# Kernel tuning notes

Hardware: AMD Instinct MI355X
Metric: run time of the kernel (lower is better)

Reference implementation:

```python
import jax, jax.numpy as jnp
import numpy as np

BATCH = 4096
IN_DIM = 2048      # pooled CNN feature dim
OUT_DIM = 14951    # landmark classes
EPS = 1e-12        # tf.nn.l2_normalize epsilon


def _hadamard_slice(rows, cols):
    # Sylvester Hadamard entry: H[i, j] = (-1)^popcount(i & j).
    # Builds only the [rows, cols] slice of the 16384x16384 matrix.
    i = jnp.arange(rows, dtype=jnp.uint32)[:, None]
    j = jnp.arange(cols, dtype=jnp.uint32)[None, :]
    par = jax.lax.population_count(i & j) & 1
    return 1.0 - 2.0 * par.astype(jnp.float32)


def setup_inputs() -> dict:
    key = jax.random.key(0)
    k1, k2 = jax.random.split(key)
    x = jax.random.normal(k1, (BATCH, IN_DIM), dtype=jnp.float32)
    init_scale = 1.0 / np.sqrt(OUT_DIM)
    scale = jnp.full((1,), init_scale, dtype=jnp.float32)
    bias = jax.random.uniform(k2, (OUT_DIM,), dtype=jnp.float32,
                              minval=-init_scale, maxval=init_scale)
    return {"x": x, "scale": scale, "bias": bias}


def reference(x, scale, bias):
    H = _hadamard_slice(x.shape[1], bias.shape[0])  # [IN_DIM, OUT_DIM], +-1
    # L2-normalize along last axis (matches K.l2_normalize / tf.nn.l2_normalize)
    xn = x * jax.lax.rsqrt(jnp.maximum(jnp.sum(x * x, axis=-1, keepdims=True), EPS))
    out = -scale * jnp.matmul(xn, H) + bias  # activation=None
    return out
```

## Files before the change

### kernel.cpp

```cpp
#include <hip/hip_runtime.h>

#define BATCH   4096
#define IN_DIM  2048
#define OUT_DIM 14951
#define ROWS    4
#define NT      512
#define STRIDE  2052
#define EPS     1e-12f

__global__ __launch_bounds__(NT, 8) void HadamardClassifier_44487271252814_kernel(
    const float* __restrict__ x,
    const float* __restrict__ scale,
    const float* __restrict__ bias,
    float* __restrict__ out)
{
    __shared__ float y[ROWS * STRIDE];
    __shared__ float rss[ROWS * 2];
    __shared__ float srow[ROWS];

    const int tid = threadIdx.x;
    const int r   = tid >> 7;
    const int t   = tid & 127;
    const int b0  = blockIdx.x * ROWS;

    const float4* xv = reinterpret_cast<const float4*>(x + (size_t)(b0 + r) * IN_DIM) + 4 * t;
    float4 v0 = xv[0], v1 = xv[1], v2 = xv[2], v3 = xv[3];
    float a[16] = { v0.x, v0.y, v0.z, v0.w, v1.x, v1.y, v1.z, v1.w,
                    v2.x, v2.y, v2.z, v2.w, v3.x, v3.y, v3.z, v3.w };

    float ss = 0.f;
    #pragma unroll
    for (int k = 0; k < 16; ++k) ss += a[k] * a[k];
    #pragma unroll
    for (int o = 32; o > 0; o >>= 1) ss += __shfl_down(ss, o, 64);
    if ((tid & 63) == 0) rss[tid >> 6] = ss;

    #pragma unroll
    for (int h = 1; h < 16; h <<= 1) {
        #pragma unroll
        for (int g = 0; g < 16; g += 2 * h) {
            #pragma unroll
            for (int k = 0; k < h; ++k) {
                float u = a[g + k], w = a[g + k + h];
                a[g + k]     = u + w;
                a[g + k + h] = u - w;
            }
        }
    }

    float* yr = y + r * STRIDE;
    #pragma unroll
    for (int k = 0; k < 4; ++k) {
        *reinterpret_cast<float4*>(&yr[16 * t + 4 * k]) =
            make_float4(a[4 * k], a[4 * k + 1], a[4 * k + 2], a[4 * k + 3]);
    }
    __syncthreads();

    if (tid < ROWS)
        srow[tid] = -scale[0] * rsqrtf(fmaxf(rss[2 * tid] + rss[2 * tid + 1], EPS));

    #pragma unroll
    for (int h = 16; h < IN_DIM; h <<= 1) {
        #pragma unroll
        for (int q = 0; q < 2; ++q) {
            int idx = 4 * (t + 128 * q);
            int i = ((idx & ~(h - 1)) << 1) | (idx & (h - 1));
            float4 u = *reinterpret_cast<float4*>(&yr[i]);
            float4 w = *reinterpret_cast<float4*>(&yr[i + h]);
            float4 su, sw;
            su.x = u.x + w.x; su.y = u.y + w.y; su.z = u.z + w.z; su.w = u.w + w.w;
            sw.x = u.x - w.x; sw.y = u.y - w.y; sw.z = u.z - w.z; sw.w = u.w - w.w;
            *reinterpret_cast<float4*>(&yr[i])     = su;
            *reinterpret_cast<float4*>(&yr[i + h]) = sw;
        }
        __syncthreads();
    }

    float4* obase = reinterpret_cast<float4*>(out + (size_t)b0 * OUT_DIM);
    const int NF4 = (ROWS * OUT_DIM) / 4;

    for (int f4 = tid; f4 < NF4; f4 += NT) {
        int e  = f4 << 2;
        int rr = (e >= OUT_DIM) + (e >= 2 * OUT_DIM) + (e >= 3 * OUT_DIM);
        int j  = e - rr * OUT_DIM;
        float4 o;
        if (j + 3 < OUT_DIM) {
            float sv = srow[rr];
            const float* yq = y + rr * STRIDE;
            int m = j & (IN_DIM - 1);
            float y0 = yq[m];
            float y1 = yq[(m + 1) & (IN_DIM - 1)];
            float y2 = yq[(m + 2) & (IN_DIM - 1)];
            float y3 = yq[(m + 3) & (IN_DIM - 1)];
            o.x = fmaf(sv, y0, bias[j]);
            o.y = fmaf(sv, y1, bias[j + 1]);
            o.z = fmaf(sv, y2, bias[j + 2]);
            o.w = fmaf(sv, y3, bias[j + 3]);
        } else {
            float tmp[4];
            #pragma unroll
            for (int c = 0; c < 4; ++c) {
                int ee = e + c;
                int rc = (ee >= OUT_DIM) + (ee >= 2 * OUT_DIM) + (ee >= 3 * OUT_DIM);
                int jc = ee - rc * OUT_DIM;
                tmp[c] = fmaf(srow[rc], y[rc * STRIDE + (jc & (IN_DIM - 1))], bias[jc]);
            }
            o = make_float4(tmp[0], tmp[1], tmp[2], tmp[3]);
        }
        obase[f4] = o;
    }
}

extern "C" void kernel_launch(void* const* d_in, const int* in_sizes, int n_in,
                              void* d_out, int out_size, void* d_ws, size_t ws_size,
                              hipStream_t stream) {
    const float* x     = (const float*)d_in[0];
    const float* scale = (const float*)d_in[1];
    const float* bias  = (const float*)d_in[2];
    float* out = (float*)d_out;

    hipLaunchKernelGGL(HadamardClassifier_44487271252814_kernel,
                       dim3(BATCH / ROWS), dim3(NT), 0, stream,
                       x, scale, bias, out);
}
```

Baseline: 288.8 us.

## Use wave shuffles for FWHT stages and vectorize row-aligned output stores

Replaces the shared-memory butterfly stages h=16..1024 with in-register shfl_xor stages across the wavefront and a single shared-memory exchange for the final stage. This cuts the number of block barriers. The output loop is restructured so each iteration writes four aligned float4s, one per row, with per-row shifted reads of the transform and bias. It uses nontemporal stores and handles the few misaligned edge elements separately. The rewrite is meant to remove the scalar LDS gathers, the per-element row/column index math, and the cache pollution caused by the large output write.

```diff
diff --git a/kernel.cpp b/kernel.cpp
--- a/kernel.cpp
+++ b/kernel.cpp
@@ -7,6 +7,8 @@
 #define NT      512
 #define STRIDE  2052
 #define EPS     1e-12f
+
+typedef float nfloat4 __attribute__((ext_vector_type(4)));
 
 __global__ __launch_bounds__(NT, 8) void HadamardClassifier_44487271252814_kernel(
     const float* __restrict__ x,
@@ -32,7 +34,7 @@
     #pragma unroll
     for (int k = 0; k < 16; ++k) ss += a[k] * a[k];
     #pragma unroll
-    for (int o = 32; o > 0; o >>= 1) ss += __shfl_down(ss, o, 64);
+    for (int off = 32; off > 0; off >>= 1) ss += __shfl_down(ss, off, 64);
     if ((tid & 63) == 0) rss[tid >> 6] = ss;
 
     #pragma unroll
@@ -48,66 +50,107 @@
         }
     }
 
+    #pragma unroll
+    for (int s = 0; s < 6; ++s) {
+        const float sgn = (t & (1 << s)) ? -1.0f : 1.0f;
+        #pragma unroll
+        for (int k = 0; k < 16; ++k) {
+            float recv = __shfl_xor(a[k], 1 << s, 64);
+            a[k] = fmaf(sgn, a[k], recv);
+        }
+    }
+
     float* yr = y + r * STRIDE;
     #pragma unroll
-    for (int k = 0; k < 4; ++k) {
+    for (int k = 0; k < 4; ++k)
         *reinterpret_cast<float4*>(&yr[16 * t + 4 * k]) =
             make_float4(a[4 * k], a[4 * k + 1], a[4 * k + 2], a[4 * k + 3]);
-    }
     __syncthreads();
 
     if (tid < ROWS)
         srow[tid] = -scale[0] * rsqrtf(fmaxf(rss[2 * tid] + rss[2 * tid + 1], EPS));
 
+    const int tp = t ^ 64;
+    float p[16];
     #pragma unroll
-    for (int h = 16; h < IN_DIM; h <<= 1) {
-        #pragma unroll
-        for (int q = 0; q < 2; ++q) {
-            int idx = 4 * (t + 128 * q);
-            int i = ((idx & ~(h - 1)) << 1) | (idx & (h - 1));
-            float4 u = *reinterpret_cast<float4*>(&yr[i]);
-            float4 w = *reinterpret_cast<float4*>(&yr[i + h]);
-            float4 su, sw;
-            su.x = u.x + w.x; su.y = u.y + w.y; su.z = u.z + w.z; su.w = u.w + w.w;
-            sw.x = u.x - w.x; sw.y = u.y - w.y; sw.z = u.z - w.z; sw.w = u.w - w.w;
-            *reinterpret_cast<float4*>(&yr[i])     = su;
-            *reinterpret_cast<float4*>(&yr[i + h]) = sw;
+    for (int k = 0; k < 4; ++k) {
+        float4 w = *reinterpret_cast<const float4*>(&yr[16 * tp + 4 * k]);
+        p[4 * k] = w.x; p[4 * k + 1] = w.y; p[4 * k + 2] = w.z; p[4 * k + 3] = w.w;
+    }
+    __syncthreads();
+
+    const float sg = (t < 64) ? 1.0f : -1.0f;
+    #pragma unroll
+    for (int k = 0; k < 16; ++k) a[k] = fmaf(sg, a[k], p[k]);
+
+    #pragma unroll
+    for (int k = 0; k < 4; ++k)
+        *reinterpret_cast<float4*>(&yr[16 * t + 4 * k]) =
+            make_float4(a[4 * k], a[4 * k + 1], a[4 * k + 2], a[4 * k + 3]);
+    if (t == 0)
+        *reinterpret_cast<float4*>(&yr[2048]) = make_float4(a[0], a[1], a[2], a[3]);
+    __syncthreads();
+
+    const float sv0 = srow[0], sv1 = srow[1], sv2 = srow[2], sv3 = srow[3];
+    const float* y0p = y;
+    const float* y1p = y + STRIDE;
+    const float* y2p = y + 2 * STRIDE;
+    const float* y3p = y + 3 * STRIDE;
+
+    for (int k = tid; k < (OUT_DIM >> 2) - 1; k += NT) {
+        const int e  = 4 * k;
+        const int m4 = e & (IN_DIM - 1);
+        const float4 blo = *reinterpret_cast<const float4*>(&bias[e]);
+        const float4 bhi = *reinterpret_cast<const float4*>(&bias[e + 4]);
+        const size_t ob = (size_t)b0 * OUT_DIM + e;
+
+        {
+            const float4 w0 = *reinterpret_cast<const float4*>(&y0p[m4]);
+            nfloat4 o;
+            o.x = fmaf(sv0, w0.x, blo.x);
+            o.y = fmaf(sv0, w0.y, blo.y);
+            o.z = fmaf(sv0, w0.z, blo.z);
+            o.w = fmaf(sv0, w0.w, blo.w);
+            __builtin_nontemporal_store(o, reinterpret_cast<nfloat4*>(&out[ob]));
         }
-        __syncthreads();
+        {
+            const float4 w0 = *reinterpret_cast<const float4*>(&y1p[m4]);
+            const float4 w1 = *reinterpret_cast<const float4*>(&y1p[m4 + 4]);
+            nfloat4 o;
+            o.x = fmaf(sv1, w0.y, blo.y);
+            o.y = fmaf(sv1, w0.z, blo.z);
+            o.z = fmaf(sv1, w0.w, blo.w);
+            o.w = fmaf(sv1, w1.x, bhi.x);
+            __builtin_nontemporal_store(o, reinterpret_cast<nfloat4*>(&out[ob + OUT_DIM + 1]));
+        }
+        {
+            const float4 w0 = *reinterpret_cast<const float4*>(&y2p[m4]);
+            const float4 w1 = *reinterpret_cast<const float4*>(&y2p[m4 + 4]);
+            nfloat4 o;
+            o.x = fmaf(sv2, w0.z, blo.z);
+            o.y = fmaf(sv2, w0.w, blo.w);
+            o.z = fmaf(sv2, w1.x, bhi.x);
+            o.w = fmaf(sv2, w1.y, bhi.y);
+            __builtin_nontemporal_store(o, reinterpret_cast<nfloat4*>(&out[ob + 2 * OUT_DIM + 2]));
+        }
+        {
+            const float4 w0 = *reinterpret_cast<const float4*>(&y3p[m4]);
+            const float4 w1 = *reinterpret_cast<const float4*>(&y3p[m4 + 4]);
+            nfloat4 o;
+            o.x = fmaf(sv3, w0.w, blo.w);
+            o.y = fmaf(sv3, w1.x, bhi.x);
+            o.z = fmaf(sv3, w1.y, bhi.y);
+            o.w = fmaf(sv3, w1.z, bhi.z);
+            __builtin_nontemporal_store(o, reinterpret_cast<nfloat4*>(&out[ob + 3 * OUT_DIM + 3]));
+        }
     }
 
-    float4* obase = reinterpret_cast<float4*>(out + (size_t)b0 * OUT_DIM);
-    const int NF4 = (ROWS * OUT_DIM) / 4;
-
-    for (int f4 = tid; f4 < NF4; f4 += NT) {
-        int e  = f4 << 2;
-        int rr = (e >= OUT_DIM) + (e >= 2 * OUT_DIM) + (e >= 3 * OUT_DIM);
-        int j  = e - rr * OUT_DIM;
-        float4 o;
-        if (j + 3 < OUT_DIM) {
-            float sv = srow[rr];
-            const float* yq = y + rr * STRIDE;
-            int m = j & (IN_DIM - 1);
-            float y0 = yq[m];
-            float y1 = yq[(m + 1) & (IN_DIM - 1)];
-            float y2 = yq[(m + 2) & (IN_DIM - 1)];
-            float y3 = yq[(m + 3) & (IN_DIM - 1)];
-            o.x = fmaf(sv, y0, bias[j]);
-            o.y = fmaf(sv, y1, bias[j + 1]);
-            o.z = fmaf(sv, y2, bias[j + 2]);
-            o.w = fmaf(sv, y3, bias[j + 3]);
-        } else {
-            float tmp[4];
-            #pragma unroll
-            for (int c = 0; c < 4; ++c) {
-                int ee = e + c;
-                int rc = (ee >= OUT_DIM) + (ee >= 2 * OUT_DIM) + (ee >= 3 * OUT_DIM);
-                int jc = ee - rc * OUT_DIM;
-                tmp[c] = fmaf(srow[rc], y[rc * STRIDE + (jc & (IN_DIM - 1))], bias[jc]);
-            }
-            o = make_float4(tmp[0], tmp[1], tmp[2], tmp[3]);
-        }
-        obase[f4] = o;
+    if (tid < 28) {
+        const int rr  = tid / 7;
+        const int idx = tid - rr * 7;
+        const int j   = (idx < rr) ? idx : (14944 + idx);
+        out[(size_t)(b0 + rr) * OUT_DIM + j] =
+            fmaf(srow[rr], y[rr * STRIDE + (j & (IN_DIM - 1))], bias[j]);
     }
 }
 
```

After: 289.8 us. Within noise of the previous version (+0.3%).
